# Kernel tuning notes

Hardware: AMD Instinct MI355X
Metric: run time of the kernel (lower is better)

The kernel has to match this reference:

```python
import jax, jax.numpy as jnp
import numpy as np

T, B, I, H = 1024, 32, 512, 512


def setup_inputs() -> dict:
    key = jax.random.key(0)
    k1, k2, k3, k4, k5 = jax.random.split(key, 5)
    s = 1.0 / np.sqrt(H)
    return {
        "input_": jax.random.normal(k1, (T, B, I), dtype=jnp.float32),
        "h0": jnp.zeros((B, H), dtype=jnp.float32),
        "c0": jnp.zeros((B, H), dtype=jnp.float32),
        "W_ih": jax.random.normal(k2, (4 * H, I), dtype=jnp.float32) * s,
        "W_hh": jax.random.normal(k3, (4 * H, H), dtype=jnp.float32) * s,
        "b_ih": jax.random.normal(k4, (4 * H,), dtype=jnp.float32) * s,
        "b_hh": jax.random.normal(k5, (4 * H,), dtype=jnp.float32) * s,
    }


def _lstm_scan(input_, h0, c0, W_ih, W_hh, b_ih, b_hh):
    # Precompute input projections for all timesteps: [T, B, 4H]
    gates_x = jnp.einsum("tbi,gi->tbg", input_, W_ih) + b_ih + b_hh
    hdim = h0.shape[-1]

    def step(carry, gx):
        h, c = carry
        gates = gx + h @ W_hh.T  # [B, 4H]
        i_g, f_g, g_g, o_g = jnp.split(gates, 4, axis=-1)
        i_g = jax.nn.sigmoid(i_g)
        f_g = jax.nn.sigmoid(f_g)
        g_g = jnp.tanh(g_g)
        o_g = jax.nn.sigmoid(o_g)
        c_new = f_g * c + i_g * g_g
        h_new = o_g * jnp.tanh(c_new)
        return (h_new, c_new), h_new

    (h_f, c_f), outputs = jax.lax.scan(step, (h0, c0), gates_x)
    return outputs, h_f, c_f


def reference(input_, h0, c0, W_ih, W_hh, b_ih, b_hh):
    outputs, h_f, c_f = _lstm_scan(input_, h0, c0, W_ih, W_hh, b_ih, b_hh)
    return outputs, (h_f, c_f)
```

## Files before the change

### kernel.cpp

```cpp
#include <hip/hip_runtime.h>
#include <stdint.h>


#define T_STEPS 1024
#define BATCH   32
#define IDIM    512
#define HDIM    512

#define BG      4
#define JG      64
#define NBLK    (BG*JG)
#define BPB     (BATCH/BG)
#define JPB     (HDIM/JG)
#define RPB     (4*JPB)
#define NTHR    512
#define PSTRIDE 257
#define RING_D  4
#define HWORDS  (BPB*HDIM)
#define WPT     (HWORDS/NTHR)

__device__ __forceinline__ float sigmoid_f(float v) {
    return 1.0f / (1.0f + __expf(-v));
}
__device__ __forceinline__ float tanh_f(float v) {
    float e = __expf(2.0f * v);
    return 1.0f - 2.0f / (e + 1.0f);
}

__global__ __launch_bounds__(NTHR, 1) void lstm_persistent(
    const float* __restrict__ x,
    const float* __restrict__ h0,
    const float* __restrict__ c0,
    const float* __restrict__ Wih,
    const float* __restrict__ Whh,
    const float* __restrict__ bih,
    const float* __restrict__ bhh,
    float* __restrict__ out,
    unsigned long long* __restrict__ ring)
{
    __shared__ __align__(16) float xtile[BPB * IDIM];
    __shared__ __align__(16) float htile[BPB * HDIM];
    __shared__ float part[RPB * PSTRIDE];
    __shared__ float garr[RPB * 9];
    __shared__ float biasl[RPB];

    const int tid = threadIdx.x;
    const int bid = blockIdx.x;
    const int bg  = bid >> 6;
    const int jg  = bid & 63;
    const int ks  = tid >> 4;
    const int rp  = tid & 15;

    float4 wih[2][4], whh[2][4];
    #pragma unroll
    for (int r = 0; r < 2; ++r) {
        const int lr = rp * 2 + r;
        const int grow = (lr >> 3) * HDIM + jg * JPB + (lr & 7);
        const float* wi = Wih + (size_t)grow * IDIM;
        const float* wh = Whh + (size_t)grow * HDIM;
        #pragma unroll
        for (int j = 0; j < 4; ++j) {
            const int k = ks * 4 + j * 128;
            wih[r][j] = *(const float4*)(wi + k);
            whh[r][j] = *(const float4*)(wh + k);
        }
    }
    if (tid < RPB) {
        const int grow = (tid >> 3) * HDIM + jg * JPB + (tid & 7);
        biasl[tid] = bih[grow] + bhh[grow];
    }

    const int ab = tid >> 3;
    const int j1 = tid & 7;
    float cst = 0.f, hl = 0.f;
    if (tid < 64) {
        cst = c0[(size_t)(bg * BPB + ab) * HDIM + jg * JPB + j1];
    }
    __syncthreads();

    for (int t = 0; t < T_STEPS; ++t) {
        {
            const float* xsrc = x + ((size_t)t * BATCH + bg * BPB) * IDIM;
            #pragma unroll
            for (int i = 0; i < 2; ++i) {
                const int f = i * 2048 + tid * 4;
                *(float4*)(xtile + f) = *(const float4*)(xsrc + f);
            }
        }
        __syncthreads();

        unsigned long long v[WPT];
        const unsigned int tag = (unsigned int)t;
        const unsigned long long* rb =
            ring + ((size_t)((t - 1) & 3) * BG + bg) * HWORDS;
        if (t > 0) {
            #pragma unroll
            for (int w = 0; w < WPT; ++w)
                v[w] = __hip_atomic_load(rb + w * NTHR + tid,
                                         __ATOMIC_RELAXED,
                                         __HIP_MEMORY_SCOPE_AGENT);
        }

        float acc[2][BPB];
        #pragma unroll
        for (int r = 0; r < 2; ++r)
            #pragma unroll
            for (int b = 0; b < BPB; ++b) acc[r][b] = 0.0f;

        #pragma unroll
        for (int j = 0; j < 4; ++j) {
            #pragma unroll
            for (int b = 0; b < BPB; ++b) {
                const float4 vx = *(const float4*)(xtile + b * IDIM + ks * 4 + j * 128);
                #pragma unroll
                for (int r = 0; r < 2; ++r) {
                    acc[r][b] = fmaf(wih[r][j].x, vx.x, acc[r][b]);
                    acc[r][b] = fmaf(wih[r][j].y, vx.y, acc[r][b]);
                    acc[r][b] = fmaf(wih[r][j].z, vx.z, acc[r][b]);
                    acc[r][b] = fmaf(wih[r][j].w, vx.w, acc[r][b]);
                }
            }
        }

        if (t > 0) {
            for (int sweep = 0; sweep < 30000; ++sweep) {
                bool ok = true;
                #pragma unroll
                for (int w = 0; w < WPT; ++w) {
                    if ((unsigned int)v[w] != tag) {
                        v[w] = __hip_atomic_load(rb + w * NTHR + tid,
                                                 __ATOMIC_RELAXED,
                                                 __HIP_MEMORY_SCOPE_AGENT);
                        ok = false;
                    }
                }
                if (ok) break;
                __builtin_amdgcn_s_sleep(1);
            }
            #pragma unroll
            for (int w = 0; w < WPT; ++w)
                htile[w * NTHR + tid] =
                    __uint_as_float((unsigned int)(v[w] >> 32));
        } else {
            const float* hsrc = h0 + (size_t)bg * BPB * HDIM;
            #pragma unroll
            for (int i = 0; i < 2; ++i) {
                const int f = i * 2048 + tid * 4;
                *(float4*)(htile + f) = *(const float4*)(hsrc + f);
            }
        }
        __syncthreads();

        #pragma unroll
        for (int j = 0; j < 4; ++j) {
            #pragma unroll
            for (int b = 0; b < BPB; ++b) {
                const float4 vh = *(const float4*)(htile + b * HDIM + ks * 4 + j * 128);
                #pragma unroll
                for (int r = 0; r < 2; ++r) {
                    acc[r][b] = fmaf(whh[r][j].x, vh.x, acc[r][b]);
                    acc[r][b] = fmaf(whh[r][j].y, vh.y, acc[r][b]);
                    acc[r][b] = fmaf(whh[r][j].z, vh.z, acc[r][b]);
                    acc[r][b] = fmaf(whh[r][j].w, vh.w, acc[r][b]);
                }
            }
        }

        #pragma unroll
        for (int r = 0; r < 2; ++r) {
            const int lr = rp * 2 + r;
            #pragma unroll
            for (int b = 0; b < BPB; ++b)
                part[lr * PSTRIDE + b * 32 + ks] = acc[r][b];
        }
        __syncthreads();

        if (tid < 256) {
            const int b  = tid >> 5;
            const int lr = tid & 31;
            const float* p = part + lr * PSTRIDE + b * 32;
            float s0 = 0.f, s1 = 0.f, s2 = 0.f, s3 = 0.f;
            #pragma unroll
            for (int k2 = 0; k2 < 32; k2 += 4) {
                s0 += p[k2]; s1 += p[k2 + 1]; s2 += p[k2 + 2]; s3 += p[k2 + 3];
            }
            garr[lr * 9 + b] = (s0 + s1) + (s2 + s3) + biasl[lr];
        }
        __syncthreads();

        if (tid < 64) {
            const float ig = sigmoid_f(garr[(0 * 8 + j1) * 9 + ab]);
            const float fg = sigmoid_f(garr[(1 * 8 + j1) * 9 + ab]);
            const float gg = tanh_f  (garr[(2 * 8 + j1) * 9 + ab]);
            const float og = sigmoid_f(garr[(3 * 8 + j1) * 9 + ab]);
            cst = fmaf(fg, cst, ig * gg);
            hl  = og * tanh_f(cst);

            unsigned long long* rw = ring
                + ((size_t)(t & 3) * BG + bg) * HWORDS
                + ab * HDIM + jg * JPB + j1;
            __hip_atomic_store(rw,
                (((unsigned long long)__float_as_uint(hl)) << 32)
                    | (unsigned long long)(t + 1),
                __ATOMIC_RELAXED, __HIP_MEMORY_SCOPE_AGENT);

            out[((size_t)t * BATCH + bg * BPB + ab) * HDIM + jg * JPB + j1] = hl;
        }
    }

    if (tid < 64) {
        const size_t base = (size_t)T_STEPS * BATCH * HDIM;
        const size_t off  = (size_t)(bg * BPB + ab) * HDIM + jg * JPB + j1;
        out[base + off] = hl;
        out[base + (size_t)BATCH * HDIM + off] = cst;
    }
}

extern "C" void kernel_launch(void* const* d_in, const int* in_sizes, int n_in,
                              void* d_out, int out_size, void* d_ws, size_t ws_size,
                              hipStream_t stream) {
    const float* x   = (const float*)d_in[0];
    const float* h0  = (const float*)d_in[1];
    const float* c0  = (const float*)d_in[2];
    const float* Wih = (const float*)d_in[3];
    const float* Whh = (const float*)d_in[4];
    const float* bih = (const float*)d_in[5];
    const float* bhh = (const float*)d_in[6];
    float* out = (float*)d_out;
    unsigned long long* ring = (unsigned long long*)d_ws;
    lstm_persistent<<<dim3(NBLK), dim3(NTHR), 0, stream>>>(
        x, h0, c0, Wih, Whh, bih, bhh, out, ring);
}
```

Baseline: 3.742 ms.

## Double-buffer x tiles, prefetch next step, fuse gate activation via shuffles

Input tiles are now double-buffered in shared memory. The next timestep's x is loaded into registers early and written after the input projection, which removes one global load plus one __syncthreads from each step's critical path. The gate reduction and activation are fused with wave shuffles, so the garr array and another barrier are gone. An extra poll of the ring is inserted before the wait loop. The costs are more LDS use, added register pressure, and reliance on the shuffle lane mapping being correct.

```diff
diff --git a/kernel.cpp b/kernel.cpp
--- a/kernel.cpp
+++ b/kernel.cpp
@@ -38,10 +38,9 @@
     float* __restrict__ out,
     unsigned long long* __restrict__ ring)
 {
-    __shared__ __align__(16) float xtile[BPB * IDIM];
+    __shared__ __align__(16) float xtile[2][BPB * IDIM];
     __shared__ __align__(16) float htile[BPB * HDIM];
     __shared__ float part[RPB * PSTRIDE];
-    __shared__ float garr[RPB * 9];
     __shared__ float biasl[RPB];
 
     const int tid = threadIdx.x;
@@ -70,25 +69,28 @@
         biasl[tid] = bih[grow] + bhh[grow];
     }
 
-    const int ab = tid >> 3;
-    const int j1 = tid & 7;
+    const int lr_red = tid & 31;
+    const int b_red  = tid >> 5;
+    const int lid    = tid & 63;
+    const bool is_act = (tid < 256) && (lr_red < 8);
     float cst = 0.f, hl = 0.f;
-    if (tid < 64) {
-        cst = c0[(size_t)(bg * BPB + ab) * HDIM + jg * JPB + j1];
+    if (is_act) {
+        cst = c0[(size_t)(bg * BPB + b_red) * HDIM + jg * JPB + lr_red];
+    }
+
+    {
+        const float* xsrc = x + (size_t)(bg * BPB) * IDIM;
+        const float* hsrc = h0 + (size_t)bg * BPB * HDIM;
+        #pragma unroll
+        for (int i = 0; i < 2; ++i) {
+            const int f = i * 2048 + tid * 4;
+            *(float4*)(&xtile[0][f]) = *(const float4*)(xsrc + f);
+            *(float4*)(htile + f)    = *(const float4*)(hsrc + f);
+        }
     }
     __syncthreads();
 
     for (int t = 0; t < T_STEPS; ++t) {
-        {
-            const float* xsrc = x + ((size_t)t * BATCH + bg * BPB) * IDIM;
-            #pragma unroll
-            for (int i = 0; i < 2; ++i) {
-                const int f = i * 2048 + tid * 4;
-                *(float4*)(xtile + f) = *(const float4*)(xsrc + f);
-            }
-        }
-        __syncthreads();
-
         unsigned long long v[WPT];
         const unsigned int tag = (unsigned int)t;
         const unsigned long long* rb =
@@ -100,7 +102,14 @@
                                          __ATOMIC_RELAXED,
                                          __HIP_MEMORY_SCOPE_AGENT);
         }
-
+        float4 xr0, xr1;
+        if (t + 1 < T_STEPS) {
+            const float* xsrc = x + ((size_t)(t + 1) * BATCH + bg * BPB) * IDIM;
+            xr0 = *(const float4*)(xsrc + tid * 4);
+            xr1 = *(const float4*)(xsrc + 2048 + tid * 4);
+        }
+
+        const float* xt = xtile[t & 1];
         float acc[2][BPB];
         #pragma unroll
         for (int r = 0; r < 2; ++r)
@@ -111,7 +120,7 @@
         for (int j = 0; j < 4; ++j) {
             #pragma unroll
             for (int b = 0; b < BPB; ++b) {
-                const float4 vx = *(const float4*)(xtile + b * IDIM + ks * 4 + j * 128);
+                const float4 vx = *(const float4*)(xt + b * IDIM + ks * 4 + j * 128);
                 #pragma unroll
                 for (int r = 0; r < 2; ++r) {
                     acc[r][b] = fmaf(wih[r][j].x, vx.x, acc[r][b]);
@@ -120,6 +129,21 @@
                     acc[r][b] = fmaf(wih[r][j].w, vx.w, acc[r][b]);
                 }
             }
+        }
+
+        if (t > 0) {
+            #pragma unroll
+            for (int w = 0; w < WPT; ++w)
+                if ((unsigned int)v[w] != tag)
+                    v[w] = __hip_atomic_load(rb + w * NTHR + tid,
+                                             __ATOMIC_RELAXED,
+                                             __HIP_MEMORY_SCOPE_AGENT);
+        }
+
+        if (t + 1 < T_STEPS) {
+            float* xd = xtile[(t + 1) & 1];
+            *(float4*)(xd + tid * 4)        = xr0;
+            *(float4*)(xd + 2048 + tid * 4) = xr1;
         }
 
         if (t > 0) {
@@ -141,13 +165,6 @@
             for (int w = 0; w < WPT; ++w)
                 htile[w * NTHR + tid] =
                     __uint_as_float((unsigned int)(v[w] >> 32));
-        } else {
-            const float* hsrc = h0 + (size_t)bg * BPB * HDIM;
-            #pragma unroll
-            for (int i = 0; i < 2; ++i) {
-                const int f = i * 2048 + tid * 4;
-                *(float4*)(htile + f) = *(const float4*)(hsrc + f);
-            }
         }
         __syncthreads();
 
@@ -176,41 +193,44 @@
         __syncthreads();
 
         if (tid < 256) {
-            const int b  = tid >> 5;
-            const int lr = tid & 31;
-            const float* p = part + lr * PSTRIDE + b * 32;
+            const float* p = part + lr_red * PSTRIDE + b_red * 32;
             float s0 = 0.f, s1 = 0.f, s2 = 0.f, s3 = 0.f;
             #pragma unroll
             for (int k2 = 0; k2 < 32; k2 += 4) {
                 s0 += p[k2]; s1 += p[k2 + 1]; s2 += p[k2 + 2]; s3 += p[k2 + 3];
             }
-            garr[lr * 9 + b] = (s0 + s1) + (s2 + s3) + biasl[lr];
-        }
-        __syncthreads();
-
-        if (tid < 64) {
-            const float ig = sigmoid_f(garr[(0 * 8 + j1) * 9 + ab]);
-            const float fg = sigmoid_f(garr[(1 * 8 + j1) * 9 + ab]);
-            const float gg = tanh_f  (garr[(2 * 8 + j1) * 9 + ab]);
-            const float og = sigmoid_f(garr[(3 * 8 + j1) * 9 + ab]);
-            cst = fmaf(fg, cst, ig * gg);
-            hl  = og * tanh_f(cst);
-
-            unsigned long long* rw = ring
-                + ((size_t)(t & 3) * BG + bg) * HWORDS
-                + ab * HDIM + jg * JPB + j1;
-            __hip_atomic_store(rw,
-                (((unsigned long long)__float_as_uint(hl)) << 32)
-                    | (unsigned long long)(t + 1),
-                __ATOMIC_RELAXED, __HIP_MEMORY_SCOPE_AGENT);
-
-            out[((size_t)t * BATCH + bg * BPB + ab) * HDIM + jg * JPB + j1] = hl;
-        }
-    }
-
-    if (tid < 64) {
+            const float s = (s0 + s1) + (s2 + s3) + biasl[lr_red];
+
+            const int hb = lid & 32;
+            const float fs = __shfl(s, hb | ((lid + 8)  & 31), 64);
+            const float gs = __shfl(s, hb | ((lid + 16) & 31), 64);
+            const float os = __shfl(s, hb | ((lid + 24) & 31), 64);
+
+            if (lr_red < 8) {
+                const float ig = sigmoid_f(s);
+                const float fg = sigmoid_f(fs);
+                const float gg = tanh_f(gs);
+                const float og = sigmoid_f(os);
+                cst = fmaf(fg, cst, ig * gg);
+                hl  = og * tanh_f(cst);
+
+                unsigned long long* rw = ring
+                    + ((size_t)(t & 3) * BG + bg) * HWORDS
+                    + b_red * HDIM + jg * JPB + lr_red;
+                __hip_atomic_store(rw,
+                    (((unsigned long long)__float_as_uint(hl)) << 32)
+                        | (unsigned long long)(t + 1),
+                    __ATOMIC_RELAXED, __HIP_MEMORY_SCOPE_AGENT);
+
+                out[((size_t)t * BATCH + bg * BPB + b_red) * HDIM
+                    + jg * JPB + lr_red] = hl;
+            }
+        }
+    }
+
+    if (is_act) {
         const size_t base = (size_t)T_STEPS * BATCH * HDIM;
-        const size_t off  = (size_t)(bg * BPB + ab) * HDIM + jg * JPB + j1;
+        const size_t off  = (size_t)(bg * BPB + b_red) * HDIM + jg * JPB + lr_red;
         out[base + off] = hl;
         out[base + (size_t)BATCH * HDIM + off] = cst;
     }
```

New measurement: 4.941 ms. +32.1%, slower.
